# Optimization experiments

Hardware: AMD Instinct MI355X
Metric: run time of the kernel (lower is better)

Reference implementation:

```python
import jax, jax.numpy as jnp
import numpy as np

N_NODES = 50000
N_EDGES = 800000
IN_F = 129
HID = 32
HEADS = 4
N_CLS = 40
NEG_SLOPE = 0.2
BN_EPS = 1e-5


def setup_inputs() -> dict:
    key = jax.random.key(0)
    ks = jax.random.split(key, 16)
    x = jax.random.normal(ks[0], (N_NODES, IN_F), dtype=jnp.float32)
    edge_index = jax.random.randint(ks[1], (2, N_EDGES), 0, N_NODES, dtype=jnp.int64)
    # BatchNorm1d (eval mode: running stats)
    bn_gamma = jax.random.normal(ks[2], (IN_F,), dtype=jnp.float32) * 0.1 + 1.0
    bn_beta = jax.random.normal(ks[3], (IN_F,), dtype=jnp.float32) * 0.1
    bn_mean = jax.random.normal(ks[4], (IN_F,), dtype=jnp.float32) * 0.1
    bn_var = jax.random.uniform(ks[5], (IN_F,), dtype=jnp.float32, minval=0.5, maxval=1.5)
    # GATConv 1: in=129 -> heads*hid
    s1 = 1.0 / np.sqrt(IN_F)
    W1 = jax.random.uniform(ks[6], (IN_F, HEADS * HID), dtype=jnp.float32, minval=-s1, maxval=s1)
    a1_src = jax.random.uniform(ks[7], (HEADS, HID), dtype=jnp.float32, minval=-s1, maxval=s1)
    a1_dst = jax.random.uniform(ks[8], (HEADS, HID), dtype=jnp.float32, minval=-s1, maxval=s1)
    b1 = jnp.zeros((HEADS * HID,), dtype=jnp.float32)
    # GATConv 2: in=heads*hid -> heads*n_cls (concat=True default)
    in2 = HEADS * HID
    s2 = 1.0 / np.sqrt(in2)
    W2 = jax.random.uniform(ks[9], (in2, HEADS * N_CLS), dtype=jnp.float32, minval=-s2, maxval=s2)
    a2_src = jax.random.uniform(ks[10], (HEADS, N_CLS), dtype=jnp.float32, minval=-s2, maxval=s2)
    a2_dst = jax.random.uniform(ks[11], (HEADS, N_CLS), dtype=jnp.float32, minval=-s2, maxval=s2)
    b2 = jnp.zeros((HEADS * N_CLS,), dtype=jnp.float32)
    return {"x": x, "edge_index": edge_index,
            "bn_gamma": bn_gamma, "bn_beta": bn_beta, "bn_mean": bn_mean, "bn_var": bn_var,
            "W1": W1, "a1_src": a1_src, "a1_dst": a1_dst, "b1": b1,
            "W2": W2, "a2_src": a2_src, "a2_dst": a2_dst, "b2": b2}


def gat_conv(x, W, a_src, a_dst, bias, src, dst, num_nodes, heads, out_ch):
    # h: [N, H, C]
    h = (x @ W).reshape(num_nodes, heads, out_ch)
    alpha_s = jnp.einsum('nhc,hc->nh', h, a_src)   # [N, H]
    alpha_d = jnp.einsum('nhc,hc->nh', h, a_dst)   # [N, H]
    e = alpha_s[src] + alpha_d[dst]                # [E, H]
    e = jnp.where(e > 0, e, NEG_SLOPE * e)         # LeakyReLU
    # segment softmax grouped by destination node
    e_max = jax.ops.segment_max(e, dst, num_segments=num_nodes)
    p = jnp.exp(e - e_max[dst])
    denom = jax.ops.segment_sum(p, dst, num_segments=num_nodes)
    alpha = p / denom[dst]                         # [E, H]
    msg = h[src] * alpha[:, :, None]               # [E, H, C]
    out = jax.ops.segment_sum(msg, dst, num_segments=num_nodes)
    return out.reshape(num_nodes, heads * out_ch) + bias


def reference(x, edge_index, bn_gamma, bn_beta, bn_mean, bn_var,
              W1, a1_src, a1_dst, b1, W2, a2_src, a2_dst, b2):
    N = x.shape[0]
    loops = jnp.arange(N, dtype=edge_index.dtype)
    src = jnp.concatenate([edge_index[0], loops])  # add self loops (PyG default)
    dst = jnp.concatenate([edge_index[1], loops])
    # BatchNorm1d eval; dropout is identity in eval
    h = (x - bn_mean) * jax.lax.rsqrt(bn_var + BN_EPS) * bn_gamma + bn_beta
    h = gat_conv(h, W1, a1_src, a1_dst, b1, src, dst, N, HEADS, HID)
    h = jax.nn.elu(h)
    h = gat_conv(h, W2, a2_src, a2_dst, b2, src, dst, N, HEADS, N_CLS)
    return h
```

## Files before the change

### kernel.cpp

```cpp
#include <hip/hip_runtime.h>

#define N_NODES 50000
#define N_EDGES 800000
#define E_TOT   (N_EDGES + N_NODES)
#define IN_F    129
#define HID     32
#define HEADS   4
#define F1      (HEADS * HID)
#define NCLS    40
#define F2      (HEADS * NCLS)
#define NEG     0.2f
#define BN_EPS  1e-5f
#define PITCH1  132
#define SCAN_NB ((N_NODES + 255) / 256)
#define LOG2E   1.4426950408889634f

__global__ __launch_bounds__(256) void gemm1_kernel(
    const float* __restrict__ x,
    const float* __restrict__ bng, const float* __restrict__ bnb,
    const float* __restrict__ bnm, const float* __restrict__ bnv,
    const float* __restrict__ W, float* __restrict__ h1) {
  __shared__ float scale[IN_F], shift[IN_F];
  __shared__ float rows[32 * PITCH1];
  int tid = threadIdx.x;
  if (tid < IN_F) {
    float sc = bng[tid] * rsqrtf(bnv[tid] + BN_EPS);
    scale[tid] = sc;
    shift[tid] = bnb[tid] - bnm[tid] * sc;
  }
  __syncthreads();
  int nb = blockIdx.x * 32;
  int nvalid = N_NODES - nb; if (nvalid > 32) nvalid = 32;
  const float* xb = x + (size_t)nb * IN_F;
  int total = nvalid * IN_F;
  for (int i = tid; i < total; i += 256) {
    int r = i / IN_F;
    int c = i - r * IN_F;
    rows[r * PITCH1 + c] = xb[i] * scale[c] + shift[c];
  }
  __syncthreads();
  int wave = tid >> 6, lane = tid & 63;
  int r0 = wave * 8;
  if (r0 >= nvalid) return;
  const float* rp[8];
#pragma unroll
  for (int i = 0; i < 8; i++) {
    int ri = r0 + i; if (ri >= nvalid) ri = nvalid - 1;
    rp[i] = &rows[ri * PITCH1];
  }
  float a0[8] = {}, a1[8] = {};
  for (int k = 0; k < 128; k += 4) {
    float4 xv[8];
#pragma unroll
    for (int i = 0; i < 8; i++) xv[i] = *(const float4*)(rp[i] + k);
    float w00 = W[(k+0)*F1 + lane],      w10 = W[(k+0)*F1 + 64 + lane];
    float w01 = W[(k+1)*F1 + lane],      w11 = W[(k+1)*F1 + 64 + lane];
    float w02 = W[(k+2)*F1 + lane],      w12 = W[(k+2)*F1 + 64 + lane];
    float w03 = W[(k+3)*F1 + lane],      w13 = W[(k+3)*F1 + 64 + lane];
#pragma unroll
    for (int i = 0; i < 8; i++) {
      a0[i] += xv[i].x*w00 + xv[i].y*w01 + xv[i].z*w02 + xv[i].w*w03;
      a1[i] += xv[i].x*w10 + xv[i].y*w11 + xv[i].z*w12 + xv[i].w*w13;
    }
  }
  {
    float w0 = W[128*F1 + lane], w1 = W[128*F1 + 64 + lane];
#pragma unroll
    for (int i = 0; i < 8; i++) { float xk = rp[i][128]; a0[i] += xk*w0; a1[i] += xk*w1; }
  }
#pragma unroll
  for (int i = 0; i < 8; i++) {
    if (r0 + i >= nvalid) break;
    size_t n = nb + r0 + i;
    h1[n * F1 + lane]      = a0[i];
    h1[n * F1 + 64 + lane] = a1[i];
  }
}

__global__ __launch_bounds__(256) void gemm2_kernel(
    const float* __restrict__ hin, const float* __restrict__ W,
    float* __restrict__ hout) {
  __shared__ float rows[32 * F1];
  int tid = threadIdx.x;
  int nb = blockIdx.x * 32;
  int nvalid = N_NODES - nb; if (nvalid > 32) nvalid = 32;
  const float4* src4 = (const float4*)(hin + (size_t)nb * F1);
  float4* dst4 = (float4*)rows;
  int tot4 = nvalid * (F1 / 4);
  for (int i = tid; i < tot4; i += 256) dst4[i] = src4[i];
  __syncthreads();
  int wave = tid >> 6, lane = tid & 63;
  int r0 = wave * 8;
  if (r0 >= nvalid) return;
  const float* rp[8];
#pragma unroll
  for (int i = 0; i < 8; i++) {
    int ri = r0 + i; if (ri >= nvalid) ri = nvalid - 1;
    rp[i] = &rows[ri * F1];
  }
  bool third = lane < 32;
  float a0[8] = {}, a1[8] = {}, a2[8] = {};
  for (int k = 0; k < F1; k += 4) {
    float4 xv[8];
#pragma unroll
    for (int i = 0; i < 8; i++) xv[i] = *(const float4*)(rp[i] + k);
    float w00 = W[(k+0)*F2 + lane], w10 = W[(k+0)*F2 + 64 + lane];
    float w01 = W[(k+1)*F2 + lane], w11 = W[(k+1)*F2 + 64 + lane];
    float w02 = W[(k+2)*F2 + lane], w12 = W[(k+2)*F2 + 64 + lane];
    float w03 = W[(k+3)*F2 + lane], w13 = W[(k+3)*F2 + 64 + lane];
    float w20 = third ? W[(k+0)*F2 + 128 + lane] : 0.f;
    float w21 = third ? W[(k+1)*F2 + 128 + lane] : 0.f;
    float w22 = third ? W[(k+2)*F2 + 128 + lane] : 0.f;
    float w23 = third ? W[(k+3)*F2 + 128 + lane] : 0.f;
#pragma unroll
    for (int i = 0; i < 8; i++) {
      a0[i] += xv[i].x*w00 + xv[i].y*w01 + xv[i].z*w02 + xv[i].w*w03;
      a1[i] += xv[i].x*w10 + xv[i].y*w11 + xv[i].z*w12 + xv[i].w*w13;
      a2[i] += xv[i].x*w20 + xv[i].y*w21 + xv[i].z*w22 + xv[i].w*w23;
    }
  }
#pragma unroll
  for (int i = 0; i < 8; i++) {
    if (r0 + i >= nvalid) break;
    size_t n = nb + r0 + i;
    hout[n * F2 + lane]      = a0[i];
    hout[n * F2 + 64 + lane] = a1[i];
    if (third) hout[n * F2 + 128 + lane] = a2[i];
  }
}

__global__ __launch_bounds__(256) void alpha1_kernel(
    const float* __restrict__ h1, const float* __restrict__ a_src,
    const float* __restrict__ a_dst, float* __restrict__ as,
    float* __restrict__ ad) {
  int t = blockIdx.x * 256 + threadIdx.x;
  if (t >= N_NODES * HEADS) return;
  int n = t >> 2, h = t & 3;
  const float* hp = h1 + (size_t)n * F1 + h * HID;
  const float* sp = a_src + h * HID;
  const float* dp = a_dst + h * HID;
  float s = 0.f, d = 0.f;
#pragma unroll
  for (int c = 0; c < HID; c++) { float v = hp[c]; s += v * sp[c]; d += v * dp[c]; }
  as[t] = s * LOG2E; ad[t] = d * LOG2E;
}

__global__ __launch_bounds__(256) void alpha2_kernel(
    const float* __restrict__ h2, const float* __restrict__ a_src,
    const float* __restrict__ a_dst, float* __restrict__ as,
    float* __restrict__ ad) {
  int t = blockIdx.x * 256 + threadIdx.x;
  if (t >= N_NODES * HEADS) return;
  int n = t >> 2, h = t & 3;
  const float* hp = h2 + (size_t)n * F2 + h * NCLS;
  const float* sp = a_src + h * NCLS;
  const float* dp = a_dst + h * NCLS;
  float s = 0.f, d = 0.f;
#pragma unroll
  for (int c = 0; c < NCLS; c++) { float v = hp[c]; s += v * sp[c]; d += v * dp[c]; }
  as[t] = s * LOG2E; ad[t] = d * LOG2E;
}

__global__ __launch_bounds__(256) void hist_kernel(
    const int* __restrict__ ei, int* __restrict__ counts) {
  int e = blockIdx.x * 256 + threadIdx.x;
  if (e >= E_TOT) return;
  int dst = (e < N_EDGES) ? ei[N_EDGES + e] : (e - N_EDGES);
  atomicAdd(&counts[dst], 1);
}

__global__ __launch_bounds__(256) void partial_kernel(
    const int* __restrict__ counts, int* __restrict__ bsum) {
  __shared__ int red[4];
  int i = blockIdx.x * 256 + threadIdx.x;
  int v = (i < N_NODES) ? counts[i] : 0;
#pragma unroll
  for (int o = 1; o < 64; o <<= 1) v += __shfl_xor(v, o);
  int lane = threadIdx.x & 63, wave = threadIdx.x >> 6;
  if (lane == 0) red[wave] = v;
  __syncthreads();
  if (threadIdx.x == 0) bsum[blockIdx.x] = red[0] + red[1] + red[2] + red[3];
}

__global__ __launch_bounds__(256) void bscan_kernel(
    const int* __restrict__ bsum, int* __restrict__ bpre) {
  __shared__ int sh[256];
  int t = threadIdx.x;
  int v = (t < SCAN_NB) ? bsum[t] : 0;
  sh[t] = v;
  __syncthreads();
  for (int o = 1; o < 256; o <<= 1) {
    int u = (t >= o) ? sh[t - o] : 0;
    __syncthreads();
    sh[t] += u;
    __syncthreads();
  }
  if (t < SCAN_NB) bpre[t] = sh[t] - v;
}

__global__ __launch_bounds__(256) void scatter_kernel(
    const int* __restrict__ counts, const int* __restrict__ bpre,
    int* __restrict__ offsets, int* __restrict__ fillpos) {
  __shared__ int sh[256];
  int t = threadIdx.x;
  int i = blockIdx.x * 256 + t;
  int v = (i < N_NODES) ? counts[i] : 0;
  sh[t] = v;
  __syncthreads();
  for (int o = 1; o < 256; o <<= 1) {
    int u = (t >= o) ? sh[t - o] : 0;
    __syncthreads();
    sh[t] += u;
    __syncthreads();
  }
  if (i < N_NODES) {
    int excl = bpre[blockIdx.x] + sh[t] - v;
    offsets[i] = excl;
    fillpos[i] = excl;
  }
  if (i == 0) offsets[N_NODES] = E_TOT;
}

__global__ __launch_bounds__(256) void fill_kernel(
    const int* __restrict__ ei, int* __restrict__ fillpos,
    int* __restrict__ csr_src) {
  int e = blockIdx.x * 256 + threadIdx.x;
  if (e >= E_TOT) return;
  int src, dst;
  if (e < N_EDGES) { src = ei[e]; dst = ei[N_EDGES + e]; }
  else { src = dst = e - N_EDGES; }
  int pos = atomicAdd(&fillpos[dst], 1);
  csr_src[pos] = src;
}

__global__ __launch_bounds__(256) void agg1_kernel(
    const float* __restrict__ h1, const float* __restrict__ as,
    const float* __restrict__ ad, const int* __restrict__ off,
    const int* __restrict__ csr, const float* __restrict__ b1,
    float* __restrict__ out) {
  int gw = (blockIdx.x * blockDim.x + threadIdx.x) >> 6;
  int lane = threadIdx.x & 63;
  if (gw >= N_NODES) return;
  int base = off[gw];
  int deg  = off[gw + 1] - base;
  int h  = lane & 3;
  int g0 = lane >> 5;
  int g1 = 2 + (lane >> 5);
  float adh = ad[gw * 4 + h];
  float s = 0.f, acc0 = 0.f, acc1 = 0.f;
  int j = 0;
  for (; j + 4 <= deg; j += 4) {
    int sr[4];
#pragma unroll
    for (int u = 0; u < 4; u++) sr[u] = csr[base + j + u];
    float av[4], x0[4], x1[4];
#pragma unroll
    for (int u = 0; u < 4; u++) av[u] = as[sr[u]*4 + h];
#pragma unroll
    for (int u = 0; u < 4; u++) {
      const float* r = h1 + (size_t)sr[u] * F1;
      x0[u] = r[lane]; x1[u] = r[64 + lane];
    }
    float w[4];
#pragma unroll
    for (int u = 0; u < 4; u++) {
      float v = av[u] + adh;
      v = fmaxf(v, NEG * v);
      w[u] = __builtin_amdgcn_exp2f(v);
      s += w[u];
    }
#pragma unroll
    for (int u = 0; u < 4; u++) {
      float w0 = __shfl(w[u], g0);
      float w1 = __shfl(w[u], g1);
      acc0 += w0 * x0[u];
      acc1 += w1 * x1[u];
    }
  }
  for (; j < deg; j++) {
    int src = csr[base + j];
    float v = as[src*4 + h] + adh;
    v = fmaxf(v, NEG * v);
    float w = __builtin_amdgcn_exp2f(v);
    s += w;
    const float* r = h1 + (size_t)src * F1;
    float w0 = __shfl(w, g0);
    float w1 = __shfl(w, g1);
    acc0 += w0 * r[lane];
    acc1 += w1 * r[64 + lane];
  }
  float s0 = __shfl(s, g0), s1 = __shfl(s, g1);
  float o0 = acc0 / s0 + b1[lane];
  float o1 = acc1 / s1 + b1[64 + lane];
  o0 = o0 > 0.f ? o0 : expm1f(o0);
  o1 = o1 > 0.f ? o1 : expm1f(o1);
  out[(size_t)gw * F1 + lane]      = o0;
  out[(size_t)gw * F1 + 64 + lane] = o1;
}

__global__ __launch_bounds__(256) void agg2_kernel(
    const float* __restrict__ h2, const float* __restrict__ as,
    const float* __restrict__ ad, const int* __restrict__ off,
    const int* __restrict__ csr, const float* __restrict__ b2,
    float* __restrict__ out) {
  int gw = (blockIdx.x * blockDim.x + threadIdx.x) >> 6;
  int lane = threadIdx.x & 63;
  if (gw >= N_NODES) return;
  int base = off[gw];
  int deg  = off[gw + 1] - base;
  int h  = lane & 3;
  int g0 = lane / NCLS;
  int g1 = (lane + 64) / NCLS;
  const int g2 = 3;
  bool third = lane < 32;
  float adh = ad[gw * 4 + h];
  float s = 0.f, acc0 = 0.f, acc1 = 0.f, acc2 = 0.f;
  int j = 0;
  for (; j + 4 <= deg; j += 4) {
    int sr[4];
#pragma unroll
    for (int u = 0; u < 4; u++) sr[u] = csr[base + j + u];
    float av[4], x0[4], x1[4], x2[4];
#pragma unroll
    for (int u = 0; u < 4; u++) av[u] = as[sr[u]*4 + h];
#pragma unroll
    for (int u = 0; u < 4; u++) {
      const float* r = h2 + (size_t)sr[u] * F2;
      x0[u] = r[lane]; x1[u] = r[64 + lane];
      x2[u] = third ? r[128 + lane] : 0.f;
    }
    float w[4];
#pragma unroll
    for (int u = 0; u < 4; u++) {
      float v = av[u] + adh;
      v = fmaxf(v, NEG * v);
      w[u] = __builtin_amdgcn_exp2f(v);
      s += w[u];
    }
#pragma unroll
    for (int u = 0; u < 4; u++) {
      float w0 = __shfl(w[u], g0);
      float w1 = __shfl(w[u], g1);
      float w2 = __shfl(w[u], g2);
      acc0 += w0 * x0[u];
      acc1 += w1 * x1[u];
      acc2 += w2 * x2[u];
    }
  }
  for (; j < deg; j++) {
    int src = csr[base + j];
    float v = as[src*4 + h] + adh;
    v = fmaxf(v, NEG * v);
    float w = __builtin_amdgcn_exp2f(v);
    s += w;
    const float* r = h2 + (size_t)src * F2;
    float x0 = r[lane], x1 = r[64 + lane];
    float x2 = third ? r[128 + lane] : 0.f;
    float w0 = __shfl(w, g0);
    float w1 = __shfl(w, g1);
    float w2 = __shfl(w, g2);
    acc0 += w0 * x0;
    acc1 += w1 * x1;
    acc2 += w2 * x2;
  }
  float s0 = __shfl(s, g0), s1 = __shfl(s, g1), s2 = __shfl(s, g2);
  out[(size_t)gw * F2 + lane]      = acc0/s0 + b2[lane];
  out[(size_t)gw * F2 + 64 + lane] = acc1/s1 + b2[64 + lane];
  if (third) out[(size_t)gw * F2 + 128 + lane] = acc2/s2 + b2[128 + lane];
}

extern "C" void kernel_launch(void* const* d_in, const int* in_sizes, int n_in,
                              void* d_out, int out_size, void* d_ws, size_t ws_size,
                              hipStream_t stream) {
  const float* x   = (const float*)d_in[0];
  const int*   ei  = (const int*)d_in[1];
  const float* bng = (const float*)d_in[2];
  const float* bnb = (const float*)d_in[3];
  const float* bnm = (const float*)d_in[4];
  const float* bnv = (const float*)d_in[5];
  const float* W1  = (const float*)d_in[6];
  const float* a1s = (const float*)d_in[7];
  const float* a1d = (const float*)d_in[8];
  const float* b1  = (const float*)d_in[9];
  const float* W2  = (const float*)d_in[10];
  const float* a2s = (const float*)d_in[11];
  const float* a2d = (const float*)d_in[12];
  const float* b2  = (const float*)d_in[13];
  float* out = (float*)d_out;

  char* ws = (char*)d_ws;
  size_t p = 0;
  auto alloc = [&](size_t bytes) -> char* {
    char* r = ws + p;
    p += (bytes + 255) & ~(size_t)255;
    return r;
  };
  float* h1   = (float*)alloc(sizeof(float) * (size_t)N_NODES * F1);
  float* h1a  = (float*)alloc(sizeof(float) * (size_t)N_NODES * F1);
  float* h2   = (float*)alloc(sizeof(float) * (size_t)N_NODES * F2);
  float* as1  = (float*)alloc(sizeof(float) * (size_t)N_NODES * HEADS);
  float* ad1  = (float*)alloc(sizeof(float) * (size_t)N_NODES * HEADS);
  float* as2  = (float*)alloc(sizeof(float) * (size_t)N_NODES * HEADS);
  float* ad2  = (float*)alloc(sizeof(float) * (size_t)N_NODES * HEADS);
  int* counts = (int*)alloc(sizeof(int) * (N_NODES + 1));
  int* offs   = (int*)alloc(sizeof(int) * (N_NODES + 1));
  int* fpos   = (int*)alloc(sizeof(int) * N_NODES);
  int* bsum   = (int*)alloc(sizeof(int) * SCAN_NB);
  int* bpre   = (int*)alloc(sizeof(int) * SCAN_NB);
  int* csr    = (int*)alloc(sizeof(int) * E_TOT);

  hipMemsetAsync(counts, 0, sizeof(int) * (N_NODES + 1), stream);

  hist_kernel<<<(E_TOT + 255) / 256, 256, 0, stream>>>(ei, counts);
  partial_kernel<<<SCAN_NB, 256, 0, stream>>>(counts, bsum);
  bscan_kernel<<<1, 256, 0, stream>>>(bsum, bpre);
  scatter_kernel<<<SCAN_NB, 256, 0, stream>>>(counts, bpre, offs, fpos);
  fill_kernel<<<(E_TOT + 255) / 256, 256, 0, stream>>>(ei, fpos, csr);

  int gblocks = (N_NODES + 31) / 32;
  gemm1_kernel<<<gblocks, 256, 0, stream>>>(x, bng, bnb, bnm, bnv, W1, h1);
  alpha1_kernel<<<(N_NODES * HEADS + 255) / 256, 256, 0, stream>>>(h1, a1s, a1d, as1, ad1);
  agg1_kernel<<<(N_NODES + 3) / 4, 256, 0, stream>>>(h1, as1, ad1, offs, csr, b1, h1a);

  gemm2_kernel<<<gblocks, 256, 0, stream>>>(h1a, W2, h2);
  alpha2_kernel<<<(N_NODES * HEADS + 255) / 256, 256, 0, stream>>>(h2, a2s, a2d, as2, ad2);
  agg2_kernel<<<(N_NODES + 3) / 4, 256, 0, stream>>>(h2, as2, ad2, offs, csr, b2, out);
}
```

Baseline: 458.9 us.

## Gather layer-2 features as packed bf16 and vectorize feature access to float2

gemm2 now also writes a bf16-packed copy of h2 into the no-longer-needed h1 buffer, and agg2 gathers neighbour rows from it. This halves the bytes of the random per-edge gather in the second aggregation. Both GEMMs and agg1 switch to float2 per-lane column pairs, and the aggregation loops unroll over 8 edges instead of 4. The cost is bf16 rounding of the layer-2 messages, which may loosen accuracy against the fp32 reference.

New measurement: 444.7 us. 1.03x faster.

```diff
diff --git a/kernel.cpp b/kernel.cpp
--- a/kernel.cpp
+++ b/kernel.cpp
@@ -15,6 +15,13 @@
 #define SCAN_NB ((N_NODES + 255) / 256)
 #define LOG2E   1.4426950408889634f
 
+__device__ __forceinline__ unsigned pack_bf16(float lo, float hi) {
+  unsigned ul = __float_as_uint(lo), uh = __float_as_uint(hi);
+  ul = (ul + 0x7FFFu + ((ul >> 16) & 1u)) >> 16;
+  uh = (uh + 0x7FFFu + ((uh >> 16) & 1u)) >> 16;
+  return ul | (uh << 16);
+}
+
 __global__ __launch_bounds__(256) void gemm1_kernel(
     const float* __restrict__ x,
     const float* __restrict__ bng, const float* __restrict__ bnb,
@@ -53,33 +60,32 @@
     float4 xv[8];
 #pragma unroll
     for (int i = 0; i < 8; i++) xv[i] = *(const float4*)(rp[i] + k);
-    float w00 = W[(k+0)*F1 + lane],      w10 = W[(k+0)*F1 + 64 + lane];
-    float w01 = W[(k+1)*F1 + lane],      w11 = W[(k+1)*F1 + 64 + lane];
-    float w02 = W[(k+2)*F1 + lane],      w12 = W[(k+2)*F1 + 64 + lane];
-    float w03 = W[(k+3)*F1 + lane],      w13 = W[(k+3)*F1 + 64 + lane];
+    float2 w0 = *(const float2*)&W[(k+0)*F1 + 2*lane];
+    float2 w1 = *(const float2*)&W[(k+1)*F1 + 2*lane];
+    float2 w2 = *(const float2*)&W[(k+2)*F1 + 2*lane];
+    float2 w3 = *(const float2*)&W[(k+3)*F1 + 2*lane];
 #pragma unroll
     for (int i = 0; i < 8; i++) {
-      a0[i] += xv[i].x*w00 + xv[i].y*w01 + xv[i].z*w02 + xv[i].w*w03;
-      a1[i] += xv[i].x*w10 + xv[i].y*w11 + xv[i].z*w12 + xv[i].w*w13;
+      a0[i] += xv[i].x*w0.x + xv[i].y*w1.x + xv[i].z*w2.x + xv[i].w*w3.x;
+      a1[i] += xv[i].x*w0.y + xv[i].y*w1.y + xv[i].z*w2.y + xv[i].w*w3.y;
     }
   }
   {
-    float w0 = W[128*F1 + lane], w1 = W[128*F1 + 64 + lane];
-#pragma unroll
-    for (int i = 0; i < 8; i++) { float xk = rp[i][128]; a0[i] += xk*w0; a1[i] += xk*w1; }
+    float2 w = *(const float2*)&W[128*F1 + 2*lane];
+#pragma unroll
+    for (int i = 0; i < 8; i++) { float xk = rp[i][128]; a0[i] += xk*w.x; a1[i] += xk*w.y; }
   }
 #pragma unroll
   for (int i = 0; i < 8; i++) {
     if (r0 + i >= nvalid) break;
     size_t n = nb + r0 + i;
-    h1[n * F1 + lane]      = a0[i];
-    h1[n * F1 + 64 + lane] = a1[i];
+    *(float2*)&h1[n * F1 + 2*lane] = make_float2(a0[i], a1[i]);
   }
 }
 
 __global__ __launch_bounds__(256) void gemm2_kernel(
     const float* __restrict__ hin, const float* __restrict__ W,
-    float* __restrict__ hout) {
+    float* __restrict__ hout, unsigned* __restrict__ h2b) {
   __shared__ float rows[32 * F1];
   int tid = threadIdx.x;
   int nb = blockIdx.x * 32;
@@ -98,34 +104,38 @@
     int ri = r0 + i; if (ri >= nvalid) ri = nvalid - 1;
     rp[i] = &rows[ri * F1];
   }
-  bool third = lane < 32;
-  float a0[8] = {}, a1[8] = {}, a2[8] = {};
+  bool third = lane < 16;
+  float a0[8] = {}, a1[8] = {}, a2[8] = {}, a3[8] = {};
   for (int k = 0; k < F1; k += 4) {
     float4 xv[8];
 #pragma unroll
     for (int i = 0; i < 8; i++) xv[i] = *(const float4*)(rp[i] + k);
-    float w00 = W[(k+0)*F2 + lane], w10 = W[(k+0)*F2 + 64 + lane];
-    float w01 = W[(k+1)*F2 + lane], w11 = W[(k+1)*F2 + 64 + lane];
-    float w02 = W[(k+2)*F2 + lane], w12 = W[(k+2)*F2 + 64 + lane];
-    float w03 = W[(k+3)*F2 + lane], w13 = W[(k+3)*F2 + 64 + lane];
-    float w20 = third ? W[(k+0)*F2 + 128 + lane] : 0.f;
-    float w21 = third ? W[(k+1)*F2 + 128 + lane] : 0.f;
-    float w22 = third ? W[(k+2)*F2 + 128 + lane] : 0.f;
-    float w23 = third ? W[(k+3)*F2 + 128 + lane] : 0.f;
+    float2 w0 = *(const float2*)&W[(k+0)*F2 + 2*lane];
+    float2 w1 = *(const float2*)&W[(k+1)*F2 + 2*lane];
+    float2 w2 = *(const float2*)&W[(k+2)*F2 + 2*lane];
+    float2 w3 = *(const float2*)&W[(k+3)*F2 + 2*lane];
+    float2 q0 = third ? *(const float2*)&W[(k+0)*F2 + 128 + 2*lane] : make_float2(0.f,0.f);
+    float2 q1 = third ? *(const float2*)&W[(k+1)*F2 + 128 + 2*lane] : make_float2(0.f,0.f);
+    float2 q2 = third ? *(const float2*)&W[(k+2)*F2 + 128 + 2*lane] : make_float2(0.f,0.f);
+    float2 q3 = third ? *(const float2*)&W[(k+3)*F2 + 128 + 2*lane] : make_float2(0.f,0.f);
 #pragma unroll
     for (int i = 0; i < 8; i++) {
-      a0[i] += xv[i].x*w00 + xv[i].y*w01 + xv[i].z*w02 + xv[i].w*w03;
-      a1[i] += xv[i].x*w10 + xv[i].y*w11 + xv[i].z*w12 + xv[i].w*w13;
-      a2[i] += xv[i].x*w20 + xv[i].y*w21 + xv[i].z*w22 + xv[i].w*w23;
+      a0[i] += xv[i].x*w0.x + xv[i].y*w1.x + xv[i].z*w2.x + xv[i].w*w3.x;
+      a1[i] += xv[i].x*w0.y + xv[i].y*w1.y + xv[i].z*w2.y + xv[i].w*w3.y;
+      a2[i] += xv[i].x*q0.x + xv[i].y*q1.x + xv[i].z*q2.x + xv[i].w*q3.x;
+      a3[i] += xv[i].x*q0.y + xv[i].y*q1.y + xv[i].z*q2.y + xv[i].w*q3.y;
     }
   }
 #pragma unroll
   for (int i = 0; i < 8; i++) {
     if (r0 + i >= nvalid) break;
     size_t n = nb + r0 + i;
-    hout[n * F2 + lane]      = a0[i];
-    hout[n * F2 + 64 + lane] = a1[i];
-    if (third) hout[n * F2 + 128 + lane] = a2[i];
+    *(float2*)&hout[n * F2 + 2*lane] = make_float2(a0[i], a1[i]);
+    h2b[n * (F2/2) + lane] = pack_bf16(a0[i], a1[i]);
+    if (third) {
+      *(float2*)&hout[n * F2 + 128 + 2*lane] = make_float2(a2[i], a3[i]);
+      h2b[n * (F2/2) + 64 + lane] = pack_bf16(a2[i], a3[i]);
+    }
   }
 }
 
@@ -243,38 +253,35 @@
   if (gw >= N_NODES) return;
   int base = off[gw];
   int deg  = off[gw + 1] - base;
-  int h  = lane & 3;
-  int g0 = lane >> 5;
-  int g1 = 2 + (lane >> 5);
+  int h = lane & 3;
+  int g = lane >> 4;
   float adh = ad[gw * 4 + h];
   float s = 0.f, acc0 = 0.f, acc1 = 0.f;
   int j = 0;
-  for (; j + 4 <= deg; j += 4) {
-    int sr[4];
-#pragma unroll
-    for (int u = 0; u < 4; u++) sr[u] = csr[base + j + u];
-    float av[4], x0[4], x1[4];
-#pragma unroll
-    for (int u = 0; u < 4; u++) av[u] = as[sr[u]*4 + h];
-#pragma unroll
-    for (int u = 0; u < 4; u++) {
-      const float* r = h1 + (size_t)sr[u] * F1;
-      x0[u] = r[lane]; x1[u] = r[64 + lane];
-    }
-    float w[4];
-#pragma unroll
-    for (int u = 0; u < 4; u++) {
+  for (; j + 8 <= deg; j += 8) {
+    int sr[8];
+#pragma unroll
+    for (int u = 0; u < 8; u++) sr[u] = csr[base + j + u];
+    float av[8];
+#pragma unroll
+    for (int u = 0; u < 8; u++) av[u] = as[sr[u]*4 + h];
+    float2 xv[8];
+#pragma unroll
+    for (int u = 0; u < 8; u++)
+      xv[u] = *(const float2*)(h1 + (size_t)sr[u] * F1 + 2*lane);
+    float w[8];
+#pragma unroll
+    for (int u = 0; u < 8; u++) {
       float v = av[u] + adh;
       v = fmaxf(v, NEG * v);
       w[u] = __builtin_amdgcn_exp2f(v);
       s += w[u];
     }
 #pragma unroll
-    for (int u = 0; u < 4; u++) {
-      float w0 = __shfl(w[u], g0);
-      float w1 = __shfl(w[u], g1);
-      acc0 += w0 * x0[u];
-      acc1 += w1 * x1[u];
+    for (int u = 0; u < 8; u++) {
+      float wg = __shfl(w[u], g);
+      acc0 += wg * xv[u].x;
+      acc1 += wg * xv[u].y;
     }
   }
   for (; j < deg; j++) {
@@ -283,23 +290,22 @@
     v = fmaxf(v, NEG * v);
     float w = __builtin_amdgcn_exp2f(v);
     s += w;
-    const float* r = h1 + (size_t)src * F1;
-    float w0 = __shfl(w, g0);
-    float w1 = __shfl(w, g1);
-    acc0 += w0 * r[lane];
-    acc1 += w1 * r[64 + lane];
-  }
-  float s0 = __shfl(s, g0), s1 = __shfl(s, g1);
-  float o0 = acc0 / s0 + b1[lane];
-  float o1 = acc1 / s1 + b1[64 + lane];
+    float2 xv = *(const float2*)(h1 + (size_t)src * F1 + 2*lane);
+    float wg = __shfl(w, g);
+    acc0 += wg * xv.x;
+    acc1 += wg * xv.y;
+  }
+  float sg = __shfl(s, g);
+  float2 bp = *(const float2*)&b1[2*lane];
+  float o0 = acc0 / sg + bp.x;
+  float o1 = acc1 / sg + bp.y;
   o0 = o0 > 0.f ? o0 : expm1f(o0);
   o1 = o1 > 0.f ? o1 : expm1f(o1);
-  out[(size_t)gw * F1 + lane]      = o0;
-  out[(size_t)gw * F1 + 64 + lane] = o1;
+  *(float2*)&out[(size_t)gw * F1 + 2*lane] = make_float2(o0, o1);
 }
 
 __global__ __launch_bounds__(256) void agg2_kernel(
-    const float* __restrict__ h2, const float* __restrict__ as,
+    const unsigned* __restrict__ h2b, const float* __restrict__ as,
     const float* __restrict__ ad, const int* __restrict__ off,
     const int* __restrict__ csr, const float* __restrict__ b2,
     float* __restrict__ out) {
@@ -309,42 +315,41 @@
   int base = off[gw];
   int deg  = off[gw + 1] - base;
   int h  = lane & 3;
-  int g0 = lane / NCLS;
-  int g1 = (lane + 64) / NCLS;
-  const int g2 = 3;
-  bool third = lane < 32;
+  int gA = lane / 20;
+  bool third = lane < 16;
   float adh = ad[gw * 4 + h];
-  float s = 0.f, acc0 = 0.f, acc1 = 0.f, acc2 = 0.f;
+  float s = 0.f, a0 = 0.f, a1 = 0.f, a2 = 0.f, a3 = 0.f;
   int j = 0;
-  for (; j + 4 <= deg; j += 4) {
-    int sr[4];
-#pragma unroll
-    for (int u = 0; u < 4; u++) sr[u] = csr[base + j + u];
-    float av[4], x0[4], x1[4], x2[4];
-#pragma unroll
-    for (int u = 0; u < 4; u++) av[u] = as[sr[u]*4 + h];
-#pragma unroll
-    for (int u = 0; u < 4; u++) {
-      const float* r = h2 + (size_t)sr[u] * F2;
-      x0[u] = r[lane]; x1[u] = r[64 + lane];
-      x2[u] = third ? r[128 + lane] : 0.f;
-    }
-    float w[4];
-#pragma unroll
-    for (int u = 0; u < 4; u++) {
+  for (; j + 8 <= deg; j += 8) {
+    int sr[8];
+#pragma unroll
+    for (int u = 0; u < 8; u++) sr[u] = csr[base + j + u];
+    float av[8];
+#pragma unroll
+    for (int u = 0; u < 8; u++) av[u] = as[sr[u]*4 + h];
+    unsigned ua[8], ub[8];
+#pragma unroll
+    for (int u = 0; u < 8; u++) {
+      const unsigned* r = h2b + (size_t)sr[u] * (F2/2);
+      ua[u] = r[lane];
+      ub[u] = third ? r[64 + lane] : 0u;
+    }
+    float w[8];
+#pragma unroll
+    for (int u = 0; u < 8; u++) {
       float v = av[u] + adh;
       v = fmaxf(v, NEG * v);
       w[u] = __builtin_amdgcn_exp2f(v);
       s += w[u];
     }
 #pragma unroll
-    for (int u = 0; u < 4; u++) {
-      float w0 = __shfl(w[u], g0);
-      float w1 = __shfl(w[u], g1);
-      float w2 = __shfl(w[u], g2);
-      acc0 += w0 * x0[u];
-      acc1 += w1 * x1[u];
-      acc2 += w2 * x2[u];
+    for (int u = 0; u < 8; u++) {
+      float wA = __shfl(w[u], gA);
+      float w3 = __shfl(w[u], 3);
+      a0 += wA * __uint_as_float(ua[u] << 16);
+      a1 += wA * __uint_as_float(ua[u] & 0xFFFF0000u);
+      a2 += w3 * __uint_as_float(ub[u] << 16);
+      a3 += w3 * __uint_as_float(ub[u] & 0xFFFF0000u);
     }
   }
   for (; j < deg; j++) {
@@ -353,20 +358,25 @@
     v = fmaxf(v, NEG * v);
     float w = __builtin_amdgcn_exp2f(v);
     s += w;
-    const float* r = h2 + (size_t)src * F2;
-    float x0 = r[lane], x1 = r[64 + lane];
-    float x2 = third ? r[128 + lane] : 0.f;
-    float w0 = __shfl(w, g0);
-    float w1 = __shfl(w, g1);
-    float w2 = __shfl(w, g2);
-    acc0 += w0 * x0;
-    acc1 += w1 * x1;
-    acc2 += w2 * x2;
-  }
-  float s0 = __shfl(s, g0), s1 = __shfl(s, g1), s2 = __shfl(s, g2);
-  out[(size_t)gw * F2 + lane]      = acc0/s0 + b2[lane];
-  out[(size_t)gw * F2 + 64 + lane] = acc1/s1 + b2[64 + lane];
-  if (third) out[(size_t)gw * F2 + 128 + lane] = acc2/s2 + b2[128 + lane];
+    const unsigned* r = h2b + (size_t)src * (F2/2);
+    unsigned ua = r[lane];
+    unsigned ub = third ? r[64 + lane] : 0u;
+    float wA = __shfl(w, gA);
+    float w3 = __shfl(w, 3);
+    a0 += wA * __uint_as_float(ua << 16);
+    a1 += wA * __uint_as_float(ua & 0xFFFF0000u);
+    a2 += w3 * __uint_as_float(ub << 16);
+    a3 += w3 * __uint_as_float(ub & 0xFFFF0000u);
+  }
+  float sA = __shfl(s, gA), s3 = __shfl(s, 3);
+  float2 bp = *(const float2*)&b2[2*lane];
+  *(float2*)&out[(size_t)gw * F2 + 2*lane] =
+      make_float2(a0/sA + bp.x, a1/sA + bp.y);
+  if (third) {
+    float2 bq = *(const float2*)&b2[128 + 2*lane];
+    *(float2*)&out[(size_t)gw * F2 + 128 + 2*lane] =
+        make_float2(a2/s3 + bq.x, a3/s3 + bq.y);
+  }
 }
 
 extern "C" void kernel_launch(void* const* d_in, const int* in_sizes, int n_in,
@@ -408,6 +418,7 @@
   int* bsum   = (int*)alloc(sizeof(int) * SCAN_NB);
   int* bpre   = (int*)alloc(sizeof(int) * SCAN_NB);
   int* csr    = (int*)alloc(sizeof(int) * E_TOT);
+  unsigned* h2b = (unsigned*)h1;
 
   hipMemsetAsync(counts, 0, sizeof(int) * (N_NODES + 1), stream);
 
@@ -422,7 +433,7 @@
   alpha1_kernel<<<(N_NODES * HEADS + 255) / 256, 256, 0, stream>>>(h1, a1s, a1d, as1, ad1);
   agg1_kernel<<<(N_NODES + 3) / 4, 256, 0, stream>>>(h1, as1, ad1, offs, csr, b1, h1a);
 
-  gemm2_kernel<<<gblocks, 256, 0, stream>>>(h1a, W2, h2);
+  gemm2_kernel<<<gblocks, 256, 0, stream>>>(h1a, W2, h2, h2b);
   alpha2_kernel<<<(N_NODES * HEADS + 255) / 256, 256, 0, stream>>>(h2, a2s, a2d, as2, ad2);
-  agg2_kernel<<<(N_NODES + 3) / 4, 256, 0, stream>>>(h2, as2, ad2, offs, csr, b2, out);
-}
+  agg2_kernel<<<(N_NODES + 3) / 4, 256, 0, stream>>>(h2b, as2, ad2, offs, csr, b2, out);
+}
```
